# Performance work log

Hardware: AMD Instinct MI355X
Metric: run time of the kernel (lower is better)

## Reference

```python
import jax, jax.numpy as jnp
import numpy as np
from jax import lax

N = 10000      # nodes (also LSTM seq_len, batch=1)
E = 640000     # edges
D = 256        # num_node_features
H = 512        # hidden_size (GIN out / LSTM input)
LH = 512       # lstm_hidden_size
BN_EPS = 1e-5


def setup_inputs() -> dict:
    key = jax.random.key(0)
    ks = jax.random.split(key, 20)
    def lin(k, out_d, in_d):
        s = 1.0 / np.sqrt(in_d)
        return jax.random.uniform(k, (out_d, in_d), jnp.float32, -s, s)
    def vec(k, d, fan):
        s = 1.0 / np.sqrt(fan)
        return jax.random.uniform(k, (d,), jnp.float32, -s, s)
    inp = {
        "x": jax.random.normal(ks[0], (N, D), jnp.float32),
        "edge_index": jax.random.randint(ks[1], (2, E), 0, N, jnp.int64),
        # GIN MLP: Linear(D,H) -> ReLU -> Linear(H,H)
        "w1": lin(ks[2], H, D), "b1": vec(ks[3], H, D),
        "w2": lin(ks[4], H, H), "b2": vec(ks[5], H, H),
        # BatchNorm1d(H) affine params (training-mode batch stats)
        "gamma": jnp.ones((H,), jnp.float32), "beta": jnp.zeros((H,), jnp.float32),
        # LSTM layer 0 (input H) and layer 1 (input LH); torch gate order i,f,g,o
        "w_ih0": lin(ks[6], 4 * LH, H), "w_hh0": lin(ks[7], 4 * LH, LH),
        "b_ih0": vec(ks[8], 4 * LH, LH), "b_hh0": vec(ks[9], 4 * LH, LH),
        "w_ih1": lin(ks[10], 4 * LH, LH), "w_hh1": lin(ks[11], 4 * LH, LH),
        "b_ih1": vec(ks[12], 4 * LH, LH), "b_hh1": vec(ks[13], 4 * LH, LH),
        # fc head
        "fc_w": lin(ks[14], 1, LH), "fc_b": vec(ks[15], 1, LH),
    }
    return inp


def _lstm_layer(xs, w_ih, w_hh, b_ih, b_hh):
    # xs: [T, in]; batch=1 squeezed. Precompute input projection as one big GEMM.
    Hh = w_hh.shape[1]
    pre = xs @ w_ih.T + b_ih + b_hh  # [T, 4H]
    def step(carry, p):
        h, c = carry
        gates = p + h @ w_hh.T
        i, f, g, o = jnp.split(gates, 4)
        i = jax.nn.sigmoid(i); f = jax.nn.sigmoid(f)
        g = jnp.tanh(g); o = jax.nn.sigmoid(o)
        c = f * c + i * g
        h = o * jnp.tanh(c)
        return (h, c), h
    init = (jnp.zeros((Hh,), xs.dtype), jnp.zeros((Hh,), xs.dtype))
    (h, c), hs = lax.scan(step, init, pre)
    return hs, h, c


def reference(x, edge_index, w1, b1, w2, b2, gamma, beta,
              w_ih0, w_hh0, b_ih0, b_hh0, w_ih1, w_hh1, b_ih1, b_hh1,
              fc_w, fc_b):
    n = x.shape[0]
    src, dst = edge_index[0], edge_index[1]
    # GINConv, eps=0: h_i = MLP(x_i + sum_{j->i} x_j)
    agg = jax.ops.segment_sum(x[src], dst, num_segments=n)
    h = x + agg
    h = jax.nn.relu(h @ w1.T + b1) @ w2.T + b2  # [N, H]
    # BatchNorm1d, training mode: biased batch stats over nodes
    mean = h.mean(axis=0)
    var = h.var(axis=0)
    h = (h - mean) * lax.rsqrt(var + BN_EPS) * gamma + beta
    h = jax.nn.relu(h)
    # dropout(p=0.5) treated as identity (eval mode, deterministic reference)
    # LSTM over the node sequence (batch=1), 2 stacked layers
    hs0, h0, c0 = _lstm_layer(h, w_ih0, w_hh0, b_ih0, b_hh0)
    hs1, h1, c1 = _lstm_layer(hs0, w_ih1, w_hh1, b_ih1, b_hh1)
    out = hs1 @ fc_w.T + fc_b          # [N, 1]
    out = out[:, 0][None, :]           # [1, N] after squeeze(2)
    h_n = jnp.stack([h0, h1])[:, None, :]  # [num_layers, 1, LH]
    c_n = jnp.stack([c0, c1])[:, None, :]
    return out, h_n, c_n
```

## Files before the change

### kernel.cpp

```cpp
#include <hip/hip_runtime.h>
#include <stdint.h>

#define N_NODES 10000
#define E_EDGES 640000
#define D_IN    256
#define H_DIM   512
#define K0      64
#define K1      128

typedef unsigned short ushort_t;
typedef unsigned int   uint32;

__device__ __forceinline__ float bf2f(ushort_t u) {
  union { uint32 i; float f; } v; v.i = ((uint32)u) << 16; return v.f;
}
__device__ __forceinline__ ushort_t f2bf(float f) {
  union { float f; uint32 i; } v; v.f = f;
  uint32 x = v.i;
  uint32 r = (x + 0x7FFFu + ((x >> 16) & 1u)) >> 16;
  return (ushort_t)r;
}

__device__ __forceinline__ float sigmoid_f(float x) {
  return 1.f / (1.f + __expf(-x));
}
__device__ __forceinline__ float tanh_f(float x) {
  x = fminf(10.f, fmaxf(-10.f, x));
  float e2 = __expf(2.f * x);
  return (e2 - 1.f) / (e2 + 1.f);
}

__device__ __forceinline__ float ld_agent_f(float* p) {
  return __hip_atomic_load(p, __ATOMIC_RELAXED, __HIP_MEMORY_SCOPE_AGENT);
}
__device__ __forceinline__ void st_agent_f(float* p, float v) {
  __hip_atomic_store(p, v, __ATOMIC_RELAXED, __HIP_MEMORY_SCOPE_AGENT);
}
__device__ __forceinline__ void spin_relaxed(int* p, int target) {
  int guard = 0;
  while (__hip_atomic_load(p, __ATOMIC_RELAXED, __HIP_MEMORY_SCOPE_AGENT) < target) {
    __builtin_amdgcn_s_sleep(1);
    if (++guard > 100000000) break;
  }
  __atomic_signal_fence(__ATOMIC_ACQUIRE);
}
__device__ __forceinline__ void publish_relaxed(int* p, int v) {
  __atomic_signal_fence(__ATOMIC_RELEASE);
  __builtin_amdgcn_s_waitcnt(0);
  __hip_atomic_store(p, v, __ATOMIC_RELAXED, __HIP_MEMORY_SCOPE_AGENT);
}

__global__ void k_zero(int* p) {
  p[blockIdx.x * 256 + threadIdx.x] = 0;
}

__global__ void k_detect(const int* eb, int* ctrl) {
  int v = eb[2 * (int)threadIdx.x + 1];
  if (v != 0) atomicOr(ctrl, 1);
}

__device__ __forceinline__ int edge_src(const int* eb, int flag, int e) {
  return flag ? eb[e] : eb[2 * e];
}
__device__ __forceinline__ int edge_dst(const int* eb, int flag, int e) {
  return flag ? eb[E_EDGES + e] : eb[2 * (E_EDGES + e)];
}

__global__ __launch_bounds__(256) void k_count(const int* eb, const int* ctrl, int* deg) {
  int e = blockIdx.x * 256 + threadIdx.x;
  if (e >= E_EDGES) return;
  int flag = ctrl[0];
  atomicAdd(&deg[edge_dst(eb, flag, e)], 1);
}

__global__ __launch_bounds__(1024) void k_prefix(const int* deg, int* off, int* cursor) {
  __shared__ int sums[1024];
  int tid = threadIdx.x;
  const int PER = 10;
  int base = tid * PER;
  int loc[PER];
  int s = 0;
  for (int i = 0; i < PER; i++) {
    int idx = base + i;
    int v = (idx < N_NODES) ? deg[idx] : 0;
    loc[i] = s; s += v;
  }
  sums[tid] = s;
  __syncthreads();
  for (int d = 1; d < 1024; d <<= 1) {
    int v = (tid >= d) ? sums[tid - d] : 0;
    __syncthreads();
    sums[tid] += v;
    __syncthreads();
  }
  int excl = (tid == 0) ? 0 : sums[tid - 1];
  for (int i = 0; i < PER; i++) {
    int idx = base + i;
    if (idx < N_NODES) { int o = excl + loc[i]; off[idx] = o; cursor[idx] = o; }
  }
  if (tid == 1023) off[N_NODES] = sums[1023];
}

__global__ __launch_bounds__(256) void k_fill(const int* eb, const int* ctrl, int* cursor, int* csr) {
  int e = blockIdx.x * 256 + threadIdx.x;
  if (e >= E_EDGES) return;
  int flag = ctrl[0];
  int d = edge_dst(eb, flag, e);
  int s = edge_src(eb, flag, e);
  int slot = atomicAdd(&cursor[d], 1);
  csr[slot] = s;
}

__global__ __launch_bounds__(256) void k_agg(const float* x, const int* off, const int* csr, float* h0) {
  int node = blockIdx.x;
  int f = threadIdx.x;
  float acc = x[(size_t)node * D_IN + f];
  int a = off[node], b = off[node + 1];
  for (int e = a; e < b; e++) {
    int s = csr[e];
    acc += x[(size_t)s * D_IN + f];
  }
  h0[(size_t)node * D_IN + f] = acc;
}

template<int KTOT, bool RELU, bool OUTBF16, bool TWOBIAS>
__global__ __launch_bounds__(256) void k_gemm(const float* __restrict__ A,
                                              const float* __restrict__ W,
                                              const float* __restrict__ bias1,
                                              const float* __restrict__ bias2,
                                              void* __restrict__ Cout, int M, int Ncols) {
  __shared__ float As[16][65];
  __shared__ float Ws[16][65];
  int tid = threadIdx.x;
  int tx = tid & 15, ty = tid >> 4;
  int by = blockIdx.x, bn = blockIdx.y;
  int lr  = tid >> 2;
  int lk4 = (tid & 3) * 4;
  float acc[4][4];
  #pragma unroll
  for (int i = 0; i < 4; i++)
    #pragma unroll
    for (int j = 0; j < 4; j++) acc[i][j] = 0.f;

  for (int k0 = 0; k0 < KTOT; k0 += 16) {
    int arow = by * 64 + lr;
    float4 av = make_float4(0.f, 0.f, 0.f, 0.f);
    if (arow < M) av = *(const float4*)(A + (size_t)arow * KTOT + k0 + lk4);
    As[lk4 + 0][lr] = av.x; As[lk4 + 1][lr] = av.y;
    As[lk4 + 2][lr] = av.z; As[lk4 + 3][lr] = av.w;
    float4 wv = *(const float4*)(W + (size_t)(bn * 64 + lr) * KTOT + k0 + lk4);
    Ws[lk4 + 0][lr] = wv.x; Ws[lk4 + 1][lr] = wv.y;
    Ws[lk4 + 2][lr] = wv.z; Ws[lk4 + 3][lr] = wv.w;
    __syncthreads();
    #pragma unroll
    for (int k = 0; k < 16; k++) {
      float a0 = As[k][ty], a1 = As[k][16 + ty], a2 = As[k][32 + ty], a3 = As[k][48 + ty];
      float w0 = Ws[k][tx], w1 = Ws[k][16 + tx], w2 = Ws[k][32 + tx], w3 = Ws[k][48 + tx];
      acc[0][0] += a0 * w0; acc[0][1] += a0 * w1; acc[0][2] += a0 * w2; acc[0][3] += a0 * w3;
      acc[1][0] += a1 * w0; acc[1][1] += a1 * w1; acc[1][2] += a1 * w2; acc[1][3] += a1 * w3;
      acc[2][0] += a2 * w0; acc[2][1] += a2 * w1; acc[2][2] += a2 * w2; acc[2][3] += a2 * w3;
      acc[3][0] += a3 * w0; acc[3][1] += a3 * w1; acc[3][2] += a3 * w2; acc[3][3] += a3 * w3;
    }
    __syncthreads();
  }
  float* Cf = (float*)Cout;
  ushort_t* Cb = (ushort_t*)Cout;
  #pragma unroll
  for (int i = 0; i < 4; i++) {
    int row = by * 64 + 16 * i + ty;
    if (row >= M) continue;
    #pragma unroll
    for (int j = 0; j < 4; j++) {
      int col = bn * 64 + 16 * j + tx;
      float b = bias1[col];
      if (TWOBIAS) b += bias2[col];
      float v = acc[i][j] + b;
      if (RELU) v = fmaxf(v, 0.f);
      if (OUTBF16) Cb[(size_t)row * Ncols + col] = f2bf(v);
      else         Cf[(size_t)row * Ncols + col] = v;
    }
  }
}

__global__ __launch_bounds__(256) void k_bnstats(const float* y2, float* colsum, float* colsumsq) {
  int b = blockIdx.x, tid = threadIdx.x;
  int r0 = b * 64, r1 = min(r0 + 64, N_NODES);
  float s0 = 0, q0 = 0, s1 = 0, q1 = 0;
  for (int r = r0; r < r1; r++) {
    float v0 = y2[(size_t)r * H_DIM + tid];
    float v1 = y2[(size_t)r * H_DIM + tid + 256];
    s0 += v0; q0 += v0 * v0; s1 += v1; q1 += v1 * v1;
  }
  atomicAdd(&colsum[tid], s0);        atomicAdd(&colsumsq[tid], q0);
  atomicAdd(&colsum[tid + 256], s1);  atomicAdd(&colsumsq[tid + 256], q1);
}

__global__ __launch_bounds__(256) void k_bnfin(float* colsum, float* colsumsq,
                                               const float* gamma, const float* beta) {
  int c = blockIdx.x * 256 + threadIdx.x;
  if (c >= H_DIM) return;
  float mean = colsum[c] * (1.f / N_NODES);
  float var  = colsumsq[c] * (1.f / N_NODES) - mean * mean;
  float sc = gamma[c] * rsqrtf(var + 1e-5f);
  float sh = beta[c] - mean * sc;
  colsum[c] = sc; colsumsq[c] = sh;
}

__global__ __launch_bounds__(256) void k_bnapply(float* y2, const float* sc, const float* sh) {
  size_t i = (size_t)blockIdx.x * 256 + threadIdx.x;
  int c = (int)(i & (H_DIM - 1));
  float v = y2[i] * sc[c] + sh[c];
  y2[i] = v > 0.f ? v : 0.f;
}

__global__ __launch_bounds__(256, 1) void k_lstm(const ushort_t* pre0, const float* w_hh0,
                                              const float* w_ih1, const float* w_hh1,
                                              const float* b_ih1, const float* b_hh1,
                                              float* hs0, float* hs1, int* flags0, int* flags1,
                                              float* dout) {
  __shared__ float lds_in[2][512];
  __shared__ float lds_dots[32];
  __shared__ float lds_pre[32];
  __shared__ float lds_h[8], lds_c[8];
  int tid = threadIdx.x;
  int wave = tid >> 6, lane = tid & 63;
  int kp = lane & 7;
  int r = wave * 8 + (lane >> 3);
  int wg = blockIdx.x;

  float w_reg[64];

  if (wg < K0) {
    int u0 = wg * 8;
    {
      int grow = (r >> 3) * H_DIM + u0 + (r & 7);
      const float* src = w_hh0 + (size_t)grow * H_DIM + kp * 64;
      #pragma unroll
      for (int i = 0; i < 16; i++) {
        int j0 = ((i + 2 * kp) & 15) * 4;
        float4 v = *(const float4*)(src + j0);
        w_reg[4 * i + 0] = v.x; w_reg[4 * i + 1] = v.y;
        w_reg[4 * i + 2] = v.z; w_reg[4 * i + 3] = v.w;
      }
    }
    if (tid < 8) { lds_h[tid] = 0.f; lds_c[tid] = 0.f; }
    float pf = 0.f;
    if (tid < 32)
      pf = bf2f(pre0[(tid >> 3) * H_DIM + u0 + (tid & 7)]);
    __syncthreads();

    for (int t = 0; t < N_NODES; t++) {
      if (tid < 32) lds_pre[tid] = pf;
      if (t > 0 && tid < K0) spin_relaxed(&flags0[tid * 16], t);
      __syncthreads();
      if (tid < 32 && t + 1 < N_NODES)
        pf = bf2f(pre0[(size_t)(t + 1) * 2048 + (tid >> 3) * H_DIM + u0 + (tid & 7)]);
      if (t > 0) {
        float* hp = hs0 + (size_t)(t - 1) * H_DIM;
        lds_in[0][tid]       = ld_agent_f(hp + tid);
        lds_in[0][tid + 256] = ld_agent_f(hp + tid + 256);
      }
      __syncthreads();
      if (t > 0) {
        const float* hrow = &lds_in[0][kp * 64];
        float dot = 0.f;
        #pragma unroll
        for (int i = 0; i < 16; i++) {
          int j0 = ((i + 2 * kp) & 15) * 4;
          float4 h4 = *(const float4*)(hrow + j0);
          dot += w_reg[4 * i] * h4.x + w_reg[4 * i + 1] * h4.y
               + w_reg[4 * i + 2] * h4.z + w_reg[4 * i + 3] * h4.w;
        }
        dot += __shfl_xor(dot, 1, 64);
        dot += __shfl_xor(dot, 2, 64);
        dot += __shfl_xor(dot, 4, 64);
        if (kp == 0) lds_dots[r] = dot;
      } else if (tid < 32) {
        lds_dots[tid] = 0.f;
      }
      __syncthreads();
      if (tid < 8) {
        int j = tid;
        float gi = lds_dots[j]      + lds_pre[j];
        float gf = lds_dots[8 + j]  + lds_pre[8 + j];
        float gg = lds_dots[16 + j] + lds_pre[16 + j];
        float go = lds_dots[24 + j] + lds_pre[24 + j];
        float ii = sigmoid_f(gi);
        float ff = sigmoid_f(gf);
        float g2 = tanh_f(gg);
        float oo = sigmoid_f(go);
        float c = ff * lds_c[j] + ii * g2;
        float h = oo * tanh_f(c);
        lds_c[j] = c; lds_h[j] = h;
        st_agent_f(&hs0[(size_t)t * H_DIM + u0 + j], h);
        if (t == N_NODES - 1) {
          dout[10000 + u0 + j] = h;
          dout[11024 + u0 + j] = c;
        }
      }
      if (tid == 0) publish_relaxed(&flags0[wg * 16], t + 1);
      __syncthreads();
    }
  } else {
    int wg1 = wg - K0;
    int u0 = wg1 * 4;
    int m = r >> 4;
    {
      int gj = r & 15;
      int grow = (gj >> 2) * H_DIM + u0 + (gj & 3);
      const float* src = (m ? w_hh1 : w_ih1) + (size_t)grow * H_DIM + kp * 64;
      #pragma unroll
      for (int i = 0; i < 16; i++) {
        int j0 = ((i + 2 * kp) & 15) * 4;
        float4 v = *(const float4*)(src + j0);
        w_reg[4 * i + 0] = v.x; w_reg[4 * i + 1] = v.y;
        w_reg[4 * i + 2] = v.z; w_reg[4 * i + 3] = v.w;
      }
    }
    if (tid < 16) {
      int g = tid >> 2, j = tid & 3;
      int grow = g * H_DIM + u0 + j;
      lds_pre[tid] = b_ih1[grow] + b_hh1[grow];
    }
    if (tid < 4) { lds_h[tid] = 0.f; lds_c[tid] = 0.f; }
    __syncthreads();

    for (int s = 0; s < N_NODES; s++) {
      if (tid < K0) spin_relaxed(&flags0[tid * 16], s + 1);
      else if (tid < 64 + K1 && s > 0) spin_relaxed(&flags1[(tid - 64) * 16], s);
      __syncthreads();
      {
        float* p0 = hs0 + (size_t)s * H_DIM;
        lds_in[0][tid]       = ld_agent_f(p0 + tid);
        lds_in[0][tid + 256] = ld_agent_f(p0 + tid + 256);
        if (s > 0) {
          float* p1 = hs1 + (size_t)(s - 1) * H_DIM;
          lds_in[1][tid]       = ld_agent_f(p1 + tid);
          lds_in[1][tid + 256] = ld_agent_f(p1 + tid + 256);
        }
      }
      __syncthreads();
      float dot = 0.f;
      if (m == 0 || s > 0) {
        const float* hrow = &lds_in[m][kp * 64];
        #pragma unroll
        for (int i = 0; i < 16; i++) {
          int j0 = ((i + 2 * kp) & 15) * 4;
          float4 h4 = *(const float4*)(hrow + j0);
          dot += w_reg[4 * i] * h4.x + w_reg[4 * i + 1] * h4.y
               + w_reg[4 * i + 2] * h4.z + w_reg[4 * i + 3] * h4.w;
        }
      }
      dot += __shfl_xor(dot, 1, 64);
      dot += __shfl_xor(dot, 2, 64);
      dot += __shfl_xor(dot, 4, 64);
      if (kp == 0) lds_dots[r] = dot;
      __syncthreads();
      if (tid < 4) {
        int j = tid;
        float gi = lds_dots[0 * 4 + j] + lds_dots[16 + 0 * 4 + j] + lds_pre[0 * 4 + j];
        float gf = lds_dots[1 * 4 + j] + lds_dots[16 + 1 * 4 + j] + lds_pre[1 * 4 + j];
        float gg = lds_dots[2 * 4 + j] + lds_dots[16 + 2 * 4 + j] + lds_pre[2 * 4 + j];
        float go = lds_dots[3 * 4 + j] + lds_dots[16 + 3 * 4 + j] + lds_pre[3 * 4 + j];
        float ii = sigmoid_f(gi);
        float ff = sigmoid_f(gf);
        float g2 = tanh_f(gg);
        float oo = sigmoid_f(go);
        float c = ff * lds_c[j] + ii * g2;
        float h = oo * tanh_f(c);
        lds_c[j] = c; lds_h[j] = h;
        st_agent_f(&hs1[(size_t)s * H_DIM + u0 + j], h);
        if (s == N_NODES - 1) {
          dout[10000 + 512 + u0 + j] = h;
          dout[11024 + 512 + u0 + j] = c;
        }
      }
      if (tid == 0) publish_relaxed(&flags1[wg1 * 16], s + 1);
      __syncthreads();
    }
  }
}

__global__ __launch_bounds__(256) void k_fc(const float* hs1, const float* fc_w,
                                            const float* fc_b, float* dout) {
  int row = blockIdx.x * 4 + (threadIdx.x >> 6);
  int lane = threadIdx.x & 63;
  float acc = 0.f;
  #pragma unroll
  for (int j = 0; j < 8; j++) {
    int c = lane + 64 * j;
    acc += hs1[(size_t)row * H_DIM + c] * fc_w[c];
  }
  for (int d = 32; d; d >>= 1) acc += __shfl_xor(acc, d, 64);
  if (lane == 0) dout[row] = acc + fc_b[0];
}

extern "C" void kernel_launch(void* const* d_in, const int* in_sizes, int n_in,
                              void* d_out, int out_size, void* d_ws, size_t ws_size,
                              hipStream_t stream) {
  const float* x     = (const float*)d_in[0];
  const int*   eb    = (const int*)d_in[1];
  const float* w1    = (const float*)d_in[2];
  const float* b1    = (const float*)d_in[3];
  const float* w2    = (const float*)d_in[4];
  const float* b2    = (const float*)d_in[5];
  const float* gamma = (const float*)d_in[6];
  const float* beta  = (const float*)d_in[7];
  const float* w_ih0 = (const float*)d_in[8];
  const float* w_hh0 = (const float*)d_in[9];
  const float* b_ih0 = (const float*)d_in[10];
  const float* b_hh0 = (const float*)d_in[11];
  const float* w_ih1 = (const float*)d_in[12];
  const float* w_hh1 = (const float*)d_in[13];
  const float* b_ih1 = (const float*)d_in[14];
  const float* b_hh1 = (const float*)d_in[15];
  const float* fc_w  = (const float*)d_in[16];
  const float* fc_b  = (const float*)d_in[17];
  float* dout = (float*)d_out;
  char* ws = (char*)d_ws;

  int*   ctrl     = (int*)(ws + 0);
  int*   flags0   = (int*)(ws + 256);
  int*   flags1   = (int*)(ws + 4352);
  float* colsum   = (float*)(ws + 12544);
  float* colsumsq = (float*)(ws + 14592);
  int*   deg      = (int*)(ws + 16640);
  float* h0       = (float*)(ws + 65536);
  float* y1       = (float*)(ws + 10305536);
  float* y2       = (float*)(ws + 30785536);
  ushort_t* pre0  = (ushort_t*)(ws + 51265536);
  int*   off      = (int*)(ws + 51265536);
  int*   cursor   = (int*)(ws + 51306496);
  int*   csr      = (int*)(ws + 51347456);
  float* hs0      = y1;
  float* hs1      = y2;

  k_zero<<<56, 256, 0, stream>>>((int*)ws);
  k_detect<<<1, 64, 0, stream>>>(eb, ctrl);
  k_count<<<2500, 256, 0, stream>>>(eb, ctrl, deg);
  k_prefix<<<1, 1024, 0, stream>>>(deg, off, cursor);
  k_fill<<<2500, 256, 0, stream>>>(eb, ctrl, cursor, csr);
  k_agg<<<10000, 256, 0, stream>>>(x, off, csr, h0);

  dim3 g1(157, 8);
  k_gemm<256, true,  false, false><<<g1, 256, 0, stream>>>(h0, w1, b1, nullptr, y1, N_NODES, 512);
  dim3 g2(157, 8);
  k_gemm<512, false, false, false><<<g2, 256, 0, stream>>>(y1, w2, b2, nullptr, y2, N_NODES, 512);

  k_bnstats<<<157, 256, 0, stream>>>(y2, colsum, colsumsq);
  k_bnfin<<<2, 256, 0, stream>>>(colsum, colsumsq, gamma, beta);
  k_bnapply<<<20000, 256, 0, stream>>>(y2, colsum, colsumsq);

  dim3 g3(157, 32);
  k_gemm<512, false, true, true><<<g3, 256, 0, stream>>>(y2, w_ih0, b_ih0, b_hh0, pre0, N_NODES, 2048);

  k_lstm<<<192, 256, 0, stream>>>(pre0, w_hh0, w_ih1, w_hh1, b_ih1, b_hh1,
                                  hs0, hs1, flags0, flags1, dout);
  k_fc<<<2500, 256, 0, stream>>>(hs1, fc_w, fc_b, dout);
}
```

Baseline: 29.20 ms.

## Pack LSTM hidden values with step tags in ring buffers to drop flag handshakes

Each LSTM hidden value is stored as a 64-bit word carrying the float and its step number, in 64-slot ring buffers. Consumers spin directly on the data until the tags match, which replaces the separate per-workgroup flag publish, the waitcnt and the extra barriers in every recurrent step. Gate nonlinearities are now computed in parallel across lanes and combined with shuffles, and the cell state lives in a register. Layer 0 is held back every 32 steps by layer-1 progress flags so it cannot overwrite ring slots that layer 1 has not yet read. This adds tight polling on shared cache lines and depends on 64-bit atomic stores being seen as a single unit.

```diff
diff --git a/kernel.cpp b/kernel.cpp
--- a/kernel.cpp
+++ b/kernel.cpp
@@ -7,9 +7,11 @@
 #define H_DIM   512
 #define K0      64
 #define K1      128
+#define RING    64
 
 typedef unsigned short ushort_t;
 typedef unsigned int   uint32;
+typedef unsigned long long u64;
 
 __device__ __forceinline__ float bf2f(ushort_t u) {
   union { uint32 i; float f; } v; v.i = ((uint32)u) << 16; return v.f;
@@ -30,11 +32,12 @@
   return (e2 - 1.f) / (e2 + 1.f);
 }
 
-__device__ __forceinline__ float ld_agent_f(float* p) {
+__device__ __forceinline__ u64 ld_c8(const u64* p) {
   return __hip_atomic_load(p, __ATOMIC_RELAXED, __HIP_MEMORY_SCOPE_AGENT);
 }
-__device__ __forceinline__ void st_agent_f(float* p, float v) {
-  __hip_atomic_store(p, v, __ATOMIC_RELAXED, __HIP_MEMORY_SCOPE_AGENT);
+__device__ __forceinline__ void st_c8(u64* p, float h, int flag) {
+  u64 u = ((u64)(uint32)flag << 32) | (u64)__float_as_uint(h);
+  __hip_atomic_store(p, u, __ATOMIC_RELAXED, __HIP_MEMORY_SCOPE_AGENT);
 }
 __device__ __forceinline__ void spin_relaxed(int* p, int target) {
   int guard = 0;
@@ -43,11 +46,6 @@
     if (++guard > 100000000) break;
   }
   __atomic_signal_fence(__ATOMIC_ACQUIRE);
-}
-__device__ __forceinline__ void publish_relaxed(int* p, int v) {
-  __atomic_signal_fence(__ATOMIC_RELEASE);
-  __builtin_amdgcn_s_waitcnt(0);
-  __hip_atomic_store(p, v, __ATOMIC_RELAXED, __HIP_MEMORY_SCOPE_AGENT);
 }
 
 __global__ void k_zero(int* p) {
@@ -216,12 +214,11 @@
 __global__ __launch_bounds__(256, 1) void k_lstm(const ushort_t* pre0, const float* w_hh0,
                                               const float* w_ih1, const float* w_hh1,
                                               const float* b_ih1, const float* b_hh1,
-                                              float* hs0, float* hs1, int* flags0, int* flags1,
-                                              float* dout) {
+                                              u64* hs0c, u64* hs1c, float* hs1p,
+                                              int* flags1, float* dout) {
   __shared__ float lds_in[2][512];
   __shared__ float lds_dots[32];
-  __shared__ float lds_pre[32];
-  __shared__ float lds_h[8], lds_c[8];
+  __shared__ float lds_pre[2][32];
   int tid = threadIdx.x;
   int wave = tid >> 6, lane = tid & 63;
   int kp = lane & 7;
@@ -229,6 +226,7 @@
   int wg = blockIdx.x;
 
   float w_reg[64];
+  float c_reg = 0.f;
 
   if (wg < K0) {
     int u0 = wg * 8;
@@ -243,24 +241,29 @@
         w_reg[4 * i + 2] = v.z; w_reg[4 * i + 3] = v.w;
       }
     }
-    if (tid < 8) { lds_h[tid] = 0.f; lds_c[tid] = 0.f; }
     float pf = 0.f;
     if (tid < 32)
       pf = bf2f(pre0[(tid >> 3) * H_DIM + u0 + (tid & 7)]);
-    __syncthreads();
 
     for (int t = 0; t < N_NODES; t++) {
-      if (tid < 32) lds_pre[tid] = pf;
-      if (t > 0 && tid < K0) spin_relaxed(&flags0[tid * 16], t);
+      int phase = t & 1;
+      if (t > 0) {
+        const u64* pa = hs0c + ((t - 1) & (RING - 1)) * 512 + tid;
+        const u64* pb = pa + 256;
+        u64 ua, ub; int guard = 0;
+        for (;;) {
+          ua = ld_c8(pa); ub = ld_c8(pb);
+          if (((int)(ua >> 32) == t && (int)(ub >> 32) == t) || ++guard > 100000000) break;
+        }
+        lds_in[0][tid]       = __uint_as_float((uint32)ua);
+        lds_in[0][tid + 256] = __uint_as_float((uint32)ub);
+      }
+      if (tid < 32) lds_pre[phase][tid] = pf;
       __syncthreads();
       if (tid < 32 && t + 1 < N_NODES)
         pf = bf2f(pre0[(size_t)(t + 1) * 2048 + (tid >> 3) * H_DIM + u0 + (tid & 7)]);
-      if (t > 0) {
-        float* hp = hs0 + (size_t)(t - 1) * H_DIM;
-        lds_in[0][tid]       = ld_agent_f(hp + tid);
-        lds_in[0][tid + 256] = ld_agent_f(hp + tid + 256);
-      }
-      __syncthreads();
+      if ((t & 31) == 0 && t >= RING && tid < K1)
+        spin_relaxed(&flags1[tid * 16], t - 32);
       if (t > 0) {
         const float* hrow = &lds_in[0][kp * 64];
         float dot = 0.f;
@@ -279,27 +282,27 @@
         lds_dots[tid] = 0.f;
       }
       __syncthreads();
-      if (tid < 8) {
-        int j = tid;
-        float gi = lds_dots[j]      + lds_pre[j];
-        float gf = lds_dots[8 + j]  + lds_pre[8 + j];
-        float gg = lds_dots[16 + j] + lds_pre[16 + j];
-        float go = lds_dots[24 + j] + lds_pre[24 + j];
-        float ii = sigmoid_f(gi);
-        float ff = sigmoid_f(gf);
-        float g2 = tanh_f(gg);
-        float oo = sigmoid_f(go);
-        float c = ff * lds_c[j] + ii * g2;
-        float h = oo * tanh_f(c);
-        lds_c[j] = c; lds_h[j] = h;
-        st_agent_f(&hs0[(size_t)t * H_DIM + u0 + j], h);
-        if (t == N_NODES - 1) {
-          dout[10000 + u0 + j] = h;
-          dout[11024 + u0 + j] = c;
-        }
-      }
-      if (tid == 0) publish_relaxed(&flags0[wg * 16], t + 1);
-      __syncthreads();
+      if (wave == 0) {
+        float val = 0.f;
+        if (lane < 32) {
+          float pre = lds_dots[lane] + lds_pre[phase][lane];
+          val = ((lane >> 3) == 2) ? tanh_f(pre) : sigmoid_f(pre);
+        }
+        int j = lane & 7;
+        float ii = __shfl(val, j, 64);
+        float ff = __shfl(val, 8 + j, 64);
+        float gg = __shfl(val, 16 + j, 64);
+        float oo = __shfl(val, 24 + j, 64);
+        if (lane < 8) {
+          c_reg = ff * c_reg + ii * gg;
+          float hv = oo * tanh_f(c_reg);
+          st_c8(hs0c + (t & (RING - 1)) * 512 + u0 + lane, hv, t + 1);
+          if (t == N_NODES - 1) {
+            dout[10000 + u0 + lane] = hv;
+            dout[11024 + u0 + lane] = c_reg;
+          }
+        }
+      }
     }
   } else {
     int wg1 = wg - K0;
@@ -320,29 +323,37 @@
     if (tid < 16) {
       int g = tid >> 2, j = tid & 3;
       int grow = g * H_DIM + u0 + j;
-      lds_pre[tid] = b_ih1[grow] + b_hh1[grow];
-    }
-    if (tid < 4) { lds_h[tid] = 0.f; lds_c[tid] = 0.f; }
+      lds_pre[0][tid] = b_ih1[grow] + b_hh1[grow];
+    }
     __syncthreads();
 
     for (int s = 0; s < N_NODES; s++) {
-      if (tid < K0) spin_relaxed(&flags0[tid * 16], s + 1);
-      else if (tid < 64 + K1 && s > 0) spin_relaxed(&flags1[(tid - 64) * 16], s);
+      {
+        bool need1 = (s > 0);
+        const u64* p0a = hs0c + (s & (RING - 1)) * 512 + tid;
+        const u64* p0b = p0a + 256;
+        const u64* p1a = hs1c + ((s - 1) & (RING - 1)) * 512 + tid;
+        const u64* p1b = p1a + 256;
+        u64 u0a, u0b, u1a, u1b; int guard = 0;
+        for (;;) {
+          u0a = ld_c8(p0a); u0b = ld_c8(p0b);
+          u1a = ld_c8(p1a); u1b = ld_c8(p1b);
+          bool ok0 = ((int)(u0a >> 32) == s + 1) && ((int)(u0b >> 32) == s + 1);
+          bool ok1 = !need1 || (((int)(u1a >> 32) == s) && ((int)(u1b >> 32) == s));
+          if ((ok0 && ok1) || ++guard > 100000000) break;
+        }
+        if (!need1) { u1a = 0; u1b = 0; }
+        lds_in[0][tid]       = __uint_as_float((uint32)u0a);
+        lds_in[0][tid + 256] = __uint_as_float((uint32)u0b);
+        lds_in[1][tid]       = __uint_as_float((uint32)u1a);
+        lds_in[1][tid + 256] = __uint_as_float((uint32)u1b);
+      }
       __syncthreads();
+      if (tid == 0)
+        __hip_atomic_store(&flags1[wg1 * 16], s + 1, __ATOMIC_RELAXED, __HIP_MEMORY_SCOPE_AGENT);
       {
-        float* p0 = hs0 + (size_t)s * H_DIM;
-        lds_in[0][tid]       = ld_agent_f(p0 + tid);
-        lds_in[0][tid + 256] = ld_agent_f(p0 + tid + 256);
-        if (s > 0) {
-          float* p1 = hs1 + (size_t)(s - 1) * H_DIM;
-          lds_in[1][tid]       = ld_agent_f(p1 + tid);
-          lds_in[1][tid + 256] = ld_agent_f(p1 + tid + 256);
-        }
-      }
-      __syncthreads();
-      float dot = 0.f;
-      if (m == 0 || s > 0) {
         const float* hrow = &lds_in[m][kp * 64];
+        float dot = 0.f;
         #pragma unroll
         for (int i = 0; i < 16; i++) {
           int j0 = ((i + 2 * kp) & 15) * 4;
@@ -350,33 +361,34 @@
           dot += w_reg[4 * i] * h4.x + w_reg[4 * i + 1] * h4.y
                + w_reg[4 * i + 2] * h4.z + w_reg[4 * i + 3] * h4.w;
         }
-      }
-      dot += __shfl_xor(dot, 1, 64);
-      dot += __shfl_xor(dot, 2, 64);
-      dot += __shfl_xor(dot, 4, 64);
-      if (kp == 0) lds_dots[r] = dot;
+        dot += __shfl_xor(dot, 1, 64);
+        dot += __shfl_xor(dot, 2, 64);
+        dot += __shfl_xor(dot, 4, 64);
+        if (kp == 0) lds_dots[r] = dot;
+      }
       __syncthreads();
-      if (tid < 4) {
-        int j = tid;
-        float gi = lds_dots[0 * 4 + j] + lds_dots[16 + 0 * 4 + j] + lds_pre[0 * 4 + j];
-        float gf = lds_dots[1 * 4 + j] + lds_dots[16 + 1 * 4 + j] + lds_pre[1 * 4 + j];
-        float gg = lds_dots[2 * 4 + j] + lds_dots[16 + 2 * 4 + j] + lds_pre[2 * 4 + j];
-        float go = lds_dots[3 * 4 + j] + lds_dots[16 + 3 * 4 + j] + lds_pre[3 * 4 + j];
-        float ii = sigmoid_f(gi);
-        float ff = sigmoid_f(gf);
-        float g2 = tanh_f(gg);
-        float oo = sigmoid_f(go);
-        float c = ff * lds_c[j] + ii * g2;
-        float h = oo * tanh_f(c);
-        lds_c[j] = c; lds_h[j] = h;
-        st_agent_f(&hs1[(size_t)s * H_DIM + u0 + j], h);
-        if (s == N_NODES - 1) {
-          dout[10000 + 512 + u0 + j] = h;
-          dout[11024 + 512 + u0 + j] = c;
-        }
-      }
-      if (tid == 0) publish_relaxed(&flags1[wg1 * 16], s + 1);
-      __syncthreads();
+      if (wave == 0) {
+        float val = 0.f;
+        if (lane < 16) {
+          float pre = lds_dots[lane] + lds_dots[16 + lane] + lds_pre[0][lane];
+          val = ((lane >> 2) == 2) ? tanh_f(pre) : sigmoid_f(pre);
+        }
+        int j = lane & 3;
+        float ii = __shfl(val, j, 64);
+        float ff = __shfl(val, 4 + j, 64);
+        float gg = __shfl(val, 8 + j, 64);
+        float oo = __shfl(val, 12 + j, 64);
+        if (lane < 4) {
+          c_reg = ff * c_reg + ii * gg;
+          float hv = oo * tanh_f(c_reg);
+          st_c8(hs1c + (s & (RING - 1)) * 512 + u0 + lane, hv, s + 1);
+          hs1p[(size_t)s * H_DIM + u0 + lane] = hv;
+          if (s == N_NODES - 1) {
+            dout[10512 + u0 + lane] = hv;
+            dout[11536 + u0 + lane] = c_reg;
+          }
+        }
+      }
     }
   }
 }
@@ -419,21 +431,21 @@
   float* dout = (float*)d_out;
   char* ws = (char*)d_ws;
 
-  int*   ctrl     = (int*)(ws + 0);
-  int*   flags0   = (int*)(ws + 256);
-  int*   flags1   = (int*)(ws + 4352);
-  float* colsum   = (float*)(ws + 12544);
-  float* colsumsq = (float*)(ws + 14592);
-  int*   deg      = (int*)(ws + 16640);
-  float* h0       = (float*)(ws + 65536);
-  float* y1       = (float*)(ws + 10305536);
-  float* y2       = (float*)(ws + 30785536);
-  ushort_t* pre0  = (ushort_t*)(ws + 51265536);
-  int*   off      = (int*)(ws + 51265536);
-  int*   cursor   = (int*)(ws + 51306496);
-  int*   csr      = (int*)(ws + 51347456);
-  float* hs0      = y1;
-  float* hs1      = y2;
+  int*    ctrl     = (int*)(ws + 0);
+  int*    flags1   = (int*)(ws + 256);
+  float*  colsum   = (float*)(ws + 8448);
+  float*  colsumsq = (float*)(ws + 10496);
+  int*    deg      = (int*)(ws + 12544);
+  u64*    hs0c     = (u64*)(ws + 57344);
+  u64*    hs1c     = (u64*)(ws + 319488);
+  float*  y1       = (float*)(ws + 581632);
+  float*  y2       = (float*)(ws + 21061632);
+  float*  h0       = y2;
+  ushort_t* pre0   = (ushort_t*)(ws + 41541632);
+  int*    off      = (int*)(ws + 41541632);
+  int*    cursor   = (int*)(ws + 41582080);
+  int*    csr      = (int*)(ws + 41622528);
+  float*  hs1p     = y1;
 
   k_zero<<<56, 256, 0, stream>>>((int*)ws);
   k_detect<<<1, 64, 0, stream>>>(eb, ctrl);
@@ -455,6 +467,6 @@
   k_gemm<512, false, true, true><<<g3, 256, 0, stream>>>(y2, w_ih0, b_ih0, b_hh0, pre0, N_NODES, 2048);
 
   k_lstm<<<192, 256, 0, stream>>>(pre0, w_hh0, w_ih1, w_hh1, b_ih1, b_hh1,
-                                  hs0, hs1, flags0, flags1, dout);
-  k_fc<<<2500, 256, 0, stream>>>(hs1, fc_w, fc_b, dout);
-}
+                                  hs0c, hs1c, hs1p, flags1, dout);
+  k_fc<<<2500, 256, 0, stream>>>(hs1p, fc_w, fc_b, dout);
+}
```

Result: faster. 26.20 ms (-10.3%).
